# Optimization experiments

Measured on AMD Instinct MI355X. Metric: run time of the kernel, lower is better.

## Reference

```python
import jax, jax.numpy as jnp
import numpy as np

VOCAB, EMBED, ZCH = 4096, 128, 256
B, H, W = 32, 16, 16


def setup_inputs() -> dict:
    key = jax.random.key(0)
    k1, k2, k3, k4 = jax.random.split(key, 4)
    z_e = jax.random.normal(k1, (B, ZCH, H, W), dtype=jnp.float32)
    pre_w = jax.random.normal(k2, (EMBED, ZCH), dtype=jnp.float32) * 0.02
    pre_b = jnp.zeros((EMBED,), dtype=jnp.float32)
    # codebook initialized uniform(-1/vocab, 1/vocab) like the torch module
    emb = jax.random.uniform(k3, (VOCAB, EMBED), dtype=jnp.float32,
                             minval=-1.0 / VOCAB, maxval=1.0 / VOCAB)
    post_w = jax.random.normal(k4, (ZCH, EMBED), dtype=jnp.float32) * 0.02
    post_b = jnp.zeros((ZCH,), dtype=jnp.float32)
    return {"z_e": z_e, "pre_w": pre_w, "pre_b": pre_b, "emb": emb,
            "post_w": post_w, "post_b": post_b}


def reference(z_e, pre_w, pre_b, emb, post_w, post_b):
    # pre_quant_conv: 1x1 conv == per-pixel linear, z_channels -> embed_dim
    z = jnp.einsum('bchw,ec->behw', z_e, pre_w) + pre_b[None, :, None, None]
    b, e, h, w = z.shape
    zf = z.transpose(0, 2, 3, 1).reshape(-1, e)                 # (b*h*w, e)
    # squared distance to all codebook vectors: |z|^2 + |c|^2 - 2 z.c
    dist = (jnp.sum(zf * zf, axis=1, keepdims=True)
            + jnp.sum(emb * emb, axis=1)
            - 2.0 * zf @ emb.T)                                  # (b*h*w, vocab)
    tokens = jnp.argmin(dist, axis=-1)                           # (b*h*w,)
    z_q = emb[tokens].reshape(b, h, w, e).transpose(0, 3, 1, 2)  # (b,e,h,w)
    # straight-through estimator
    dec_in = z + jax.lax.stop_gradient(z_q - z)
    # post_quant_conv: 1x1 conv embed_dim -> z_channels (decoder input)
    rec = jnp.einsum('behw,ce->bchw', dec_in, post_w) + post_b[None, :, None, None]
    return z, z_q, rec
```

## Files before the change

### kernel.cpp

```cpp
#include <hip/hip_runtime.h>
#include <hip/hip_bf16.h>
#include <cstdint>

#define NB   32
#define NC   256
#define NE   128
#define NS   256
#define NV   4096
#define NP   8192
#define NSPLIT 8

typedef unsigned short ushort_t;
typedef __attribute__((ext_vector_type(8))) short bf16x8;
typedef __attribute__((ext_vector_type(8))) unsigned short us8;
typedef __attribute__((ext_vector_type(4))) float f32x4;

__device__ __forceinline__ ushort_t f2bf(float f) {
    __hip_bfloat16 h = __float2bfloat16(f);
    ushort_t u; __builtin_memcpy(&u, &h, 2); return u;
}
__device__ __forceinline__ unsigned asu(float f) { unsigned u; __builtin_memcpy(&u,&f,4); return u; }
__device__ __forceinline__ float    asf(unsigned u) { float f; __builtin_memcpy(&f,&u,4); return f; }

__global__ __launch_bounds__(256) void pack_emb(
    const float* __restrict__ emb, ushort_t* __restrict__ Bpack,
    float* __restrict__ cnorm)
{
    const int t = threadIdx.x;
    const int v     = blockIdx.x * 32 + (t >> 3);
    const int chunk = t & 7;
    const float4* rp = (const float4*)(emb + (size_t)v * NE + chunk * 16);
    float4 x0 = rp[0], x1 = rp[1], x2 = rp[2], x3 = rp[3];
    float xs[16] = { x0.x, x0.y, x0.z, x0.w, x1.x, x1.y, x1.z, x1.w,
                     x2.x, x2.y, x2.z, x2.w, x3.x, x3.y, x3.z, x3.w };
    us8 h0, h1;
    float nn = 0.f;
#pragma unroll
    for (int j = 0; j < 8; j++) {
        nn = fmaf(xs[j], xs[j], nn);
        h0[j] = f2bf(xs[j]);
    }
#pragma unroll
    for (int j = 0; j < 8; j++) {
        nn = fmaf(xs[8 + j], xs[8 + j], nn);
        h1[j] = f2bf(xs[8 + j]);
    }
    nn += __shfl_xor(nn, 1);
    nn += __shfl_xor(nn, 2);
    nn += __shfl_xor(nn, 4);
    if (chunk == 0) cnorm[v] = 0.5f * nn;

    const int G  = v >> 4;
    const int ks = chunk >> 1;
    const int q0 = (chunk & 1) * 2;
    const int L0 = (v & 15) | (q0 << 4);
    const int L1 = (v & 15) | ((q0 + 1) << 4);
    *(us8*)(Bpack + ((size_t)G * 4 + ks) * 512 + L0 * 8) = h0;
    *(us8*)(Bpack + ((size_t)G * 4 + ks) * 512 + L1 * 8) = h1;
}

#define ZE_STR  36
#define ZL_STR  132
#define ZE_OFF  0
#define R1_OFF  0
#define R2_OFF  16896
#define ZL_OFF  36864
#define T4B_OFF 53760
#define CAND_OFF 57856
#define TOK_OFF 61952
#define SM_SIZE 62080

__global__ __launch_bounds__(512, 2) void vq_main(
    const float* __restrict__ z_e, const float* __restrict__ pre_w,
    const float* __restrict__ pre_b, const float* __restrict__ emb,
    const float* __restrict__ post_w, const float* __restrict__ post_b,
    const ushort_t* __restrict__ Bpack, const float* __restrict__ cnorm,
    float* __restrict__ out_z, float* __restrict__ out_zq,
    float* __restrict__ out_rec)
{
    __shared__ __align__(16) char smraw[SM_SIZE];
    float* ze   = (float*)(smraw + ZE_OFF);
    float* r1   = (float*)(smraw + R1_OFF);
    float* r2   = (float*)(smraw + R2_OFF);
    float* zl   = (float*)(smraw + ZL_OFF);
    float* eg   = (float*)(smraw + ZL_OFF);
    float* t4b  = (float*)(smraw + T4B_OFF);
    int*   cand = (int*)(smraw + CAND_OFF);
    int*   tok  = (int*)(smraw + TOK_OFF);

    const int t  = threadIdx.x;
    const int b  = blockIdx.x >> 3;
    const int s0 = (blockIdx.x & 7) * 32;

    for (int idx = t; idx < NC * 32; idx += 512) {
        int c = idx >> 5, i = idx & 31;
        ze[c * ZE_STR + i] = z_e[((size_t)b * NC + c) * NS + s0 + i];
    }
    __syncthreads();

    {
        const int pg = t >> 7;
        const int e  = t & 127;
        const float* wr = pre_w + (size_t)e * NC;
        float a0 = 0.f, a1 = 0.f, a2 = 0.f, a3 = 0.f;
        float a4 = 0.f, a5 = 0.f, a6 = 0.f, a7 = 0.f;
#pragma unroll 2
        for (int c = 0; c < NC; c += 4) {
            float4 w4 = *(const float4*)(wr + c);
            float4 za, zb;
            za = *(const float4*)&ze[(c + 0) * ZE_STR + pg * 8];
            zb = *(const float4*)&ze[(c + 0) * ZE_STR + pg * 8 + 4];
            a0 = fmaf(w4.x, za.x, a0); a1 = fmaf(w4.x, za.y, a1);
            a2 = fmaf(w4.x, za.z, a2); a3 = fmaf(w4.x, za.w, a3);
            a4 = fmaf(w4.x, zb.x, a4); a5 = fmaf(w4.x, zb.y, a5);
            a6 = fmaf(w4.x, zb.z, a6); a7 = fmaf(w4.x, zb.w, a7);
            za = *(const float4*)&ze[(c + 1) * ZE_STR + pg * 8];
            zb = *(const float4*)&ze[(c + 1) * ZE_STR + pg * 8 + 4];
            a0 = fmaf(w4.y, za.x, a0); a1 = fmaf(w4.y, za.y, a1);
            a2 = fmaf(w4.y, za.z, a2); a3 = fmaf(w4.y, za.w, a3);
            a4 = fmaf(w4.y, zb.x, a4); a5 = fmaf(w4.y, zb.y, a5);
            a6 = fmaf(w4.y, zb.z, a6); a7 = fmaf(w4.y, zb.w, a7);
            za = *(const float4*)&ze[(c + 2) * ZE_STR + pg * 8];
            zb = *(const float4*)&ze[(c + 2) * ZE_STR + pg * 8 + 4];
            a0 = fmaf(w4.z, za.x, a0); a1 = fmaf(w4.z, za.y, a1);
            a2 = fmaf(w4.z, za.z, a2); a3 = fmaf(w4.z, za.w, a3);
            a4 = fmaf(w4.z, zb.x, a4); a5 = fmaf(w4.z, zb.y, a5);
            a6 = fmaf(w4.z, zb.z, a6); a7 = fmaf(w4.z, zb.w, a7);
            za = *(const float4*)&ze[(c + 3) * ZE_STR + pg * 8];
            zb = *(const float4*)&ze[(c + 3) * ZE_STR + pg * 8 + 4];
            a0 = fmaf(w4.w, za.x, a0); a1 = fmaf(w4.w, za.y, a1);
            a2 = fmaf(w4.w, za.z, a2); a3 = fmaf(w4.w, za.w, a3);
            a4 = fmaf(w4.w, zb.x, a4); a5 = fmaf(w4.w, zb.y, a5);
            a6 = fmaf(w4.w, zb.z, a6); a7 = fmaf(w4.w, zb.w, a7);
        }
        const float bias = pre_b[e];
        a0 += bias; a1 += bias; a2 += bias; a3 += bias;
        a4 += bias; a5 += bias; a6 += bias; a7 += bias;
        zl[(pg * 8 + 0) * ZL_STR + e] = a0;
        zl[(pg * 8 + 1) * ZL_STR + e] = a1;
        zl[(pg * 8 + 2) * ZL_STR + e] = a2;
        zl[(pg * 8 + 3) * ZL_STR + e] = a3;
        zl[(pg * 8 + 4) * ZL_STR + e] = a4;
        zl[(pg * 8 + 5) * ZL_STR + e] = a5;
        zl[(pg * 8 + 6) * ZL_STR + e] = a6;
        zl[(pg * 8 + 7) * ZL_STR + e] = a7;
        float4 lo = { a0, a1, a2, a3 };
        float4 hi = { a4, a5, a6, a7 };
        float* dst = out_z + ((size_t)b * NE + e) * NS + s0 + pg * 8;
        *(float4*)(dst + 0) = lo;
        *(float4*)(dst + 4) = hi;
    }
    __syncthreads();

    const int wave = t >> 6, lane = t & 63;
    const int am = lane & 15, aq = lane >> 4;

    bf16x8 ah[2][4];
#pragma unroll
    for (int mt = 0; mt < 2; mt++)
#pragma unroll
        for (int ks = 0; ks < 4; ks++) {
            const unsigned* src = (const unsigned*)(zl + (mt * 16 + am) * ZL_STR + ks * 32 + aq * 8);
            union { unsigned u[4]; bf16x8 v; } pk;
#pragma unroll
            for (int pr = 0; pr < 4; pr++)
                pk.u[pr] = (src[2 * pr + 1] & 0xFFFF0000u) | (src[2 * pr] >> 16);
            ah[mt][ks] = pk.v;
        }

    const int wq = wave >> 2;
    const int wv = wave & 3;

    for (int sp = 0; sp < NSPLIT; sp += 2) {
        const int split = sp + wq;
        const int Gbase = split * 32 + wv * 8;
        float cn[8];
#pragma unroll
        for (int cgi = 0; cgi < 8; cgi++)
            cn[cgi] = cnorm[(Gbase + cgi) * 16 + am];

        float b1v[8], b2v[8];
#pragma unroll
        for (int i = 0; i < 8; i++) { b1v[i] = -1e30f; b2v[i] = -1e30f; }

        bf16x8 bh[4], bhn[4];
#pragma unroll
        for (int ks = 0; ks < 4; ks++)
            bh[ks] = *(const bf16x8*)(Bpack + ((size_t)Gbase * 4 + ks) * 512 + lane * 8);

        for (int cgi = 0; cgi < 8; cgi++) {
            if (cgi < 7) {
#pragma unroll
                for (int ks = 0; ks < 4; ks++)
                    bhn[ks] = *(const bf16x8*)(Bpack + ((size_t)(Gbase + cgi + 1) * 4 + ks) * 512 + lane * 8);
            }
            f32x4 acc[2];
#pragma unroll
            for (int mt = 0; mt < 2; mt++) acc[mt] = (f32x4){0.f, 0.f, 0.f, 0.f};
#pragma unroll
            for (int ks = 0; ks < 4; ks++)
#pragma unroll
                for (int mt = 0; mt < 2; mt++)
                    acc[mt] = __builtin_amdgcn_mfma_f32_16x16x32_bf16(ah[mt][ks], bh[ks], acc[mt], 0, 0, 0);

#pragma unroll
            for (int mt = 0; mt < 2; mt++)
#pragma unroll
                for (int reg = 0; reg < 4; reg++) {
                    const int si = mt * 4 + reg;
                    float sc = acc[mt][reg] - cn[cgi];
                    float ev = asf((asu(sc) & ~7u) | (unsigned)cgi);
                    b2v[si] = fmaxf(b2v[si], fminf(ev, b1v[si]));
                    b1v[si] = fmaxf(b1v[si], ev);
                }
#pragma unroll
            for (int ks = 0; ks < 4; ks++) bh[ks] = bhn[ks];
        }

        const int slot = wv * 16 + am;
#pragma unroll
        for (int mt = 0; mt < 2; mt++)
#pragma unroll
            for (int reg = 0; reg < 4; reg++) {
                int px = mt * 16 + aq * 4 + reg;
                r1[(wq * 64 + slot) * 33 + px] = b1v[mt * 4 + reg];
                r2[(wq * 64 + slot) * 33 + px] = b2v[mt * 4 + reg];
            }
        __syncthreads();

        if (t < 256) {
            const int wq2 = t >> 7, rem = t & 127;
            const int px = rem >> 2, ch = rem & 3;
            float t1 = -1e30f, t2 = -1e30f, t3 = -1e30f, t4 = -1e30f;
            for (int i = 0; i < 16; i++) {
                int sl = ch * 16 + i;
#pragma unroll
                for (int e = 0; e < 2; e++) {
                    float raw = e ? r2[(wq2 * 64 + sl) * 33 + px]
                                  : r1[(wq2 * 64 + sl) * 33 + px];
                    unsigned vb = asu(raw);
                    float v = asf((vb & ~511u) | ((unsigned)sl << 3) | (vb & 7u));
                    t4 = fmaxf(t4, fminf(v, t3));
                    t3 = fmaxf(t3, fminf(v, t2));
                    t2 = fmaxf(t2, fminf(v, t1));
                    t1 = fmaxf(t1, v);
                }
            }
            float* dst = t4b + ((wq2 * 32 + px) * 4 + ch) * 4;
            dst[0] = t1; dst[1] = t2; dst[2] = t3; dst[3] = t4;
        }
        __syncthreads();

        if (t < 64) {
            const int wq2 = t >> 5, px = t & 31;
            float u1 = -1e30f, u2 = -1e30f, u3 = -1e30f, u4 = -1e30f;
            for (int ch = 0; ch < 4; ch++) {
#pragma unroll
                for (int j = 0; j < 4; j++) {
                    float v = t4b[((wq2 * 32 + px) * 4 + ch) * 4 + j];
                    u4 = fmaxf(u4, fminf(v, u3));
                    u3 = fmaxf(u3, fminf(v, u2));
                    u2 = fmaxf(u2, fminf(v, u1));
                    u1 = fmaxf(u1, v);
                }
            }
            const int spw = sp + wq2;
            float uu[4] = { u1, u2, u3, u4 };
#pragma unroll
            for (int j = 0; j < 4; j++) {
                unsigned bits = asu(uu[j]) & 511u;
                int w = (int)(bits >> 7), res = (int)((bits >> 3) & 15u), cg = (int)(bits & 7u);
                cand[(spw * 32 + px) * 4 + j] = spw * 512 + (w * 8 + cg) * 16 + res;
            }
        }
        __syncthreads();
    }

    {
        const int il = t >> 4;
        const int cc = t & 15;
        double bs = -1e300; int bi = 0x7fffffff;
        const float* zr = zl + il * ZL_STR;
#pragma unroll
        for (int jj = 0; jj < 2; jj++) {
            int c2 = cc * 2 + jj;
            int split = c2 >> 2, slot = c2 & 3;
            int idx = cand[(split * 32 + il) * 4 + slot];
            const float* er = emb + (size_t)idx * NE;
            double d0 = 0.0, d1 = 0.0, d2 = 0.0, d3 = 0.0;
            double n0 = 0.0, n1 = 0.0, n2 = 0.0, n3 = 0.0;
#pragma unroll
            for (int k = 0; k < NE; k += 16) {
                float4 e0 = *(const float4*)(er + k + 0);
                float4 e1 = *(const float4*)(er + k + 4);
                float4 e2 = *(const float4*)(er + k + 8);
                float4 e3 = *(const float4*)(er + k + 12);
                float4 z0 = *(const float4*)(zr + k + 0);
                float4 z1 = *(const float4*)(zr + k + 4);
                float4 z2 = *(const float4*)(zr + k + 8);
                float4 z3 = *(const float4*)(zr + k + 12);
                d0 += (double)z0.x * e0.x; d0 += (double)z0.y * e0.y;
                d0 += (double)z0.z * e0.z; d0 += (double)z0.w * e0.w;
                d1 += (double)z1.x * e1.x; d1 += (double)z1.y * e1.y;
                d1 += (double)z1.z * e1.z; d1 += (double)z1.w * e1.w;
                d2 += (double)z2.x * e2.x; d2 += (double)z2.y * e2.y;
                d2 += (double)z2.z * e2.z; d2 += (double)z2.w * e2.w;
                d3 += (double)z3.x * e3.x; d3 += (double)z3.y * e3.y;
                d3 += (double)z3.z * e3.z; d3 += (double)z3.w * e3.w;
                n0 += (double)e0.x * e0.x; n0 += (double)e0.y * e0.y;
                n0 += (double)e0.z * e0.z; n0 += (double)e0.w * e0.w;
                n1 += (double)e1.x * e1.x; n1 += (double)e1.y * e1.y;
                n1 += (double)e1.z * e1.z; n1 += (double)e1.w * e1.w;
                n2 += (double)e2.x * e2.x; n2 += (double)e2.y * e2.y;
                n2 += (double)e2.z * e2.z; n2 += (double)e2.w * e2.w;
                n3 += (double)e3.x * e3.x; n3 += (double)e3.y * e3.y;
                n3 += (double)e3.z * e3.z; n3 += (double)e3.w * e3.w;
            }
            double sc = ((d0 + d1) + (d2 + d3)) - 0.5 * ((n0 + n1) + (n2 + n3));
            if (sc > bs || (sc == bs && idx < bi)) { bs = sc; bi = idx; }
        }
#pragma unroll
        for (int m = 1; m <= 8; m <<= 1) {
            double osc = __shfl_xor(bs, m);
            int    obi = __shfl_xor(bi, m);
            if (osc > bs || (osc == bs && obi < bi)) { bs = osc; bi = obi; }
        }
        if (cc == 0) tok[il] = bi;
    }
    __syncthreads();

    for (int idx = t; idx < 32 * 32; idx += 512) {
        int px = idx >> 5, eq = idx & 31;
        float4 v4 = *(const float4*)(emb + (size_t)tok[px] * NE + eq * 4);
        *(float4*)&eg[px * ZL_STR + eq * 4] = v4;
    }
    __syncthreads();
    for (int idx = t; idx < NE * 32; idx += 512) {
        int e = idx >> 5, i = idx & 31;
        out_zq[((size_t)b * NE + e) * NS + s0 + i] = eg[i * ZL_STR + e];
    }
    __syncthreads();

    {
        const int c  = t & 255;
        const int ph = t >> 8;
        const float* wr = post_w + (size_t)c * NE;
        const float bias = post_b[c];
#pragma unroll
        for (int pass = 0; pass < 2; pass++) {
            const int pb = pass * 16 + ph * 8;
            float a0 = 0.f, a1 = 0.f, a2 = 0.f, a3 = 0.f;
            float a4 = 0.f, a5 = 0.f, a6 = 0.f, a7 = 0.f;
#pragma unroll 4
            for (int k = 0; k < NE; k += 4) {
                float4 w4 = *(const float4*)(wr + k);
                float4 q;
                q = *(const float4*)&eg[(pb + 0) * ZL_STR + k];
                a0 = fmaf(w4.x, q.x, fmaf(w4.y, q.y, fmaf(w4.z, q.z, fmaf(w4.w, q.w, a0))));
                q = *(const float4*)&eg[(pb + 1) * ZL_STR + k];
                a1 = fmaf(w4.x, q.x, fmaf(w4.y, q.y, fmaf(w4.z, q.z, fmaf(w4.w, q.w, a1))));
                q = *(const float4*)&eg[(pb + 2) * ZL_STR + k];
                a2 = fmaf(w4.x, q.x, fmaf(w4.y, q.y, fmaf(w4.z, q.z, fmaf(w4.w, q.w, a2))));
                q = *(const float4*)&eg[(pb + 3) * ZL_STR + k];
                a3 = fmaf(w4.x, q.x, fmaf(w4.y, q.y, fmaf(w4.z, q.z, fmaf(w4.w, q.w, a3))));
                q = *(const float4*)&eg[(pb + 4) * ZL_STR + k];
                a4 = fmaf(w4.x, q.x, fmaf(w4.y, q.y, fmaf(w4.z, q.z, fmaf(w4.w, q.w, a4))));
                q = *(const float4*)&eg[(pb + 5) * ZL_STR + k];
                a5 = fmaf(w4.x, q.x, fmaf(w4.y, q.y, fmaf(w4.z, q.z, fmaf(w4.w, q.w, a5))));
                q = *(const float4*)&eg[(pb + 6) * ZL_STR + k];
                a6 = fmaf(w4.x, q.x, fmaf(w4.y, q.y, fmaf(w4.z, q.z, fmaf(w4.w, q.w, a6))));
                q = *(const float4*)&eg[(pb + 7) * ZL_STR + k];
                a7 = fmaf(w4.x, q.x, fmaf(w4.y, q.y, fmaf(w4.z, q.z, fmaf(w4.w, q.w, a7))));
            }
            float4 lo = { a0 + bias, a1 + bias, a2 + bias, a3 + bias };
            float4 hi = { a4 + bias, a5 + bias, a6 + bias, a7 + bias };
            float* dst = out_rec + ((size_t)b * NC + c) * NS + s0 + pb;
            *(float4*)(dst + 0) = lo;
            *(float4*)(dst + 4) = hi;
        }
    }
}

extern "C" void kernel_launch(void* const* d_in, const int* in_sizes, int n_in,
                              void* d_out, int out_size, void* d_ws, size_t ws_size,
                              hipStream_t stream)
{
    const float* z_e    = (const float*)d_in[0];
    const float* pre_w  = (const float*)d_in[1];
    const float* pre_b  = (const float*)d_in[2];
    const float* emb    = (const float*)d_in[3];
    const float* post_w = (const float*)d_in[4];
    const float* post_b = (const float*)d_in[5];

    float* out     = (float*)d_out;
    float* out_z   = out;
    float* out_zq  = out + 1048576;
    float* out_rec = out + 2097152;

    const size_t SZ_BPACK = (size_t)256 * 4 * 512 * 2;
    const size_t SZ_CNORM = (size_t)NV * 4;
    const size_t NEED = SZ_BPACK + SZ_CNORM;
    char* scr = (ws_size >= NEED) ? (char*)d_ws : (char*)out_rec;
    ushort_t* Bpack = (ushort_t*)scr;
    float*    cnorm = (float*)(scr + SZ_BPACK);

    pack_emb<<<dim3(128), 256, 0, stream>>>(emb, Bpack, cnorm);
    vq_main <<<dim3(256), 512, 0, stream>>>(z_e, pre_w, pre_b, emb,
                                            post_w, post_b, Bpack, cnorm,
                                            out_z, out_zq, out_rec);
}
```

Baseline: 144.4 us.

## Halve per-block pixel tile to 16 and double grid to fill more CUs

Each block now handles 16 spatial positions instead of 32, and the grid doubles to 512 blocks. The MFMA codebook scan uses a single M-tile per wave, the shared-memory reduction buffers shrink, and the candidate rerank assigns one candidate per thread. The goal is more parallelism and occupancy across CUs, at the cost of reading the packed codebook twice as often and less operand reuse per MFMA. One barrier between the z_q store and the post-conv is removed.

```diff
diff --git a/kernel.cpp b/kernel.cpp
--- a/kernel.cpp
+++ b/kernel.cpp
@@ -59,16 +59,16 @@
     *(us8*)(Bpack + ((size_t)G * 4 + ks) * 512 + L1 * 8) = h1;
 }
 
-#define ZE_STR  36
-#define ZL_STR  132
-#define ZE_OFF  0
-#define R1_OFF  0
-#define R2_OFF  16896
-#define ZL_OFF  36864
-#define T4B_OFF 53760
-#define CAND_OFF 57856
-#define TOK_OFF 61952
-#define SM_SIZE 62080
+#define ZE_STR   20
+#define ZL_STR   132
+#define ZE_OFF   0
+#define R1_OFF   0
+#define R2_OFF   8704
+#define T4B_OFF  17408
+#define ZL_OFF   20480
+#define CAND_OFF 28928
+#define TOK_OFF  30976
+#define SM_SIZE  31040
 
 __global__ __launch_bounds__(512, 2) void vq_main(
     const float* __restrict__ z_e, const float* __restrict__ pre_w,
@@ -82,19 +82,20 @@
     float* ze   = (float*)(smraw + ZE_OFF);
     float* r1   = (float*)(smraw + R1_OFF);
     float* r2   = (float*)(smraw + R2_OFF);
+    float* t4b  = (float*)(smraw + T4B_OFF);
     float* zl   = (float*)(smraw + ZL_OFF);
     float* eg   = (float*)(smraw + ZL_OFF);
-    float* t4b  = (float*)(smraw + T4B_OFF);
     int*   cand = (int*)(smraw + CAND_OFF);
     int*   tok  = (int*)(smraw + TOK_OFF);
 
     const int t  = threadIdx.x;
-    const int b  = blockIdx.x >> 3;
-    const int s0 = (blockIdx.x & 7) * 32;
-
-    for (int idx = t; idx < NC * 32; idx += 512) {
-        int c = idx >> 5, i = idx & 31;
-        ze[c * ZE_STR + i] = z_e[((size_t)b * NC + c) * NS + s0 + i];
+    const int b  = blockIdx.x >> 4;
+    const int s0 = (blockIdx.x & 15) * 16;
+
+    for (int idx = t; idx < NC * 4; idx += 512) {
+        int c = idx >> 2, q = idx & 3;
+        *(float4*)&ze[c * ZE_STR + q * 4] =
+            *(const float4*)(z_e + ((size_t)b * NC + c) * NS + s0 + q * 4);
     }
     __syncthreads();
 
@@ -103,70 +104,47 @@
         const int e  = t & 127;
         const float* wr = pre_w + (size_t)e * NC;
         float a0 = 0.f, a1 = 0.f, a2 = 0.f, a3 = 0.f;
-        float a4 = 0.f, a5 = 0.f, a6 = 0.f, a7 = 0.f;
 #pragma unroll 2
         for (int c = 0; c < NC; c += 4) {
             float4 w4 = *(const float4*)(wr + c);
-            float4 za, zb;
-            za = *(const float4*)&ze[(c + 0) * ZE_STR + pg * 8];
-            zb = *(const float4*)&ze[(c + 0) * ZE_STR + pg * 8 + 4];
-            a0 = fmaf(w4.x, za.x, a0); a1 = fmaf(w4.x, za.y, a1);
-            a2 = fmaf(w4.x, za.z, a2); a3 = fmaf(w4.x, za.w, a3);
-            a4 = fmaf(w4.x, zb.x, a4); a5 = fmaf(w4.x, zb.y, a5);
-            a6 = fmaf(w4.x, zb.z, a6); a7 = fmaf(w4.x, zb.w, a7);
-            za = *(const float4*)&ze[(c + 1) * ZE_STR + pg * 8];
-            zb = *(const float4*)&ze[(c + 1) * ZE_STR + pg * 8 + 4];
-            a0 = fmaf(w4.y, za.x, a0); a1 = fmaf(w4.y, za.y, a1);
-            a2 = fmaf(w4.y, za.z, a2); a3 = fmaf(w4.y, za.w, a3);
-            a4 = fmaf(w4.y, zb.x, a4); a5 = fmaf(w4.y, zb.y, a5);
-            a6 = fmaf(w4.y, zb.z, a6); a7 = fmaf(w4.y, zb.w, a7);
-            za = *(const float4*)&ze[(c + 2) * ZE_STR + pg * 8];
-            zb = *(const float4*)&ze[(c + 2) * ZE_STR + pg * 8 + 4];
-            a0 = fmaf(w4.z, za.x, a0); a1 = fmaf(w4.z, za.y, a1);
-            a2 = fmaf(w4.z, za.z, a2); a3 = fmaf(w4.z, za.w, a3);
-            a4 = fmaf(w4.z, zb.x, a4); a5 = fmaf(w4.z, zb.y, a5);
-            a6 = fmaf(w4.z, zb.z, a6); a7 = fmaf(w4.z, zb.w, a7);
-            za = *(const float4*)&ze[(c + 3) * ZE_STR + pg * 8];
-            zb = *(const float4*)&ze[(c + 3) * ZE_STR + pg * 8 + 4];
-            a0 = fmaf(w4.w, za.x, a0); a1 = fmaf(w4.w, za.y, a1);
-            a2 = fmaf(w4.w, za.z, a2); a3 = fmaf(w4.w, za.w, a3);
-            a4 = fmaf(w4.w, zb.x, a4); a5 = fmaf(w4.w, zb.y, a5);
-            a6 = fmaf(w4.w, zb.z, a6); a7 = fmaf(w4.w, zb.w, a7);
+            float4 z4;
+            z4 = *(const float4*)&ze[(c + 0) * ZE_STR + pg * 4];
+            a0 = fmaf(w4.x, z4.x, a0); a1 = fmaf(w4.x, z4.y, a1);
+            a2 = fmaf(w4.x, z4.z, a2); a3 = fmaf(w4.x, z4.w, a3);
+            z4 = *(const float4*)&ze[(c + 1) * ZE_STR + pg * 4];
+            a0 = fmaf(w4.y, z4.x, a0); a1 = fmaf(w4.y, z4.y, a1);
+            a2 = fmaf(w4.y, z4.z, a2); a3 = fmaf(w4.y, z4.w, a3);
+            z4 = *(const float4*)&ze[(c + 2) * ZE_STR + pg * 4];
+            a0 = fmaf(w4.z, z4.x, a0); a1 = fmaf(w4.z, z4.y, a1);
+            a2 = fmaf(w4.z, z4.z, a2); a3 = fmaf(w4.z, z4.w, a3);
+            z4 = *(const float4*)&ze[(c + 3) * ZE_STR + pg * 4];
+            a0 = fmaf(w4.w, z4.x, a0); a1 = fmaf(w4.w, z4.y, a1);
+            a2 = fmaf(w4.w, z4.z, a2); a3 = fmaf(w4.w, z4.w, a3);
         }
         const float bias = pre_b[e];
         a0 += bias; a1 += bias; a2 += bias; a3 += bias;
-        a4 += bias; a5 += bias; a6 += bias; a7 += bias;
-        zl[(pg * 8 + 0) * ZL_STR + e] = a0;
-        zl[(pg * 8 + 1) * ZL_STR + e] = a1;
-        zl[(pg * 8 + 2) * ZL_STR + e] = a2;
-        zl[(pg * 8 + 3) * ZL_STR + e] = a3;
-        zl[(pg * 8 + 4) * ZL_STR + e] = a4;
-        zl[(pg * 8 + 5) * ZL_STR + e] = a5;
-        zl[(pg * 8 + 6) * ZL_STR + e] = a6;
-        zl[(pg * 8 + 7) * ZL_STR + e] = a7;
-        float4 lo = { a0, a1, a2, a3 };
-        float4 hi = { a4, a5, a6, a7 };
-        float* dst = out_z + ((size_t)b * NE + e) * NS + s0 + pg * 8;
-        *(float4*)(dst + 0) = lo;
-        *(float4*)(dst + 4) = hi;
+        zl[(pg * 4 + 0) * ZL_STR + e] = a0;
+        zl[(pg * 4 + 1) * ZL_STR + e] = a1;
+        zl[(pg * 4 + 2) * ZL_STR + e] = a2;
+        zl[(pg * 4 + 3) * ZL_STR + e] = a3;
+        float4 o = { a0, a1, a2, a3 };
+        *(float4*)(out_z + ((size_t)b * NE + e) * NS + s0 + pg * 4) = o;
     }
     __syncthreads();
 
     const int wave = t >> 6, lane = t & 63;
     const int am = lane & 15, aq = lane >> 4;
 
-    bf16x8 ah[2][4];
-#pragma unroll
-    for (int mt = 0; mt < 2; mt++)
-#pragma unroll
-        for (int ks = 0; ks < 4; ks++) {
-            const unsigned* src = (const unsigned*)(zl + (mt * 16 + am) * ZL_STR + ks * 32 + aq * 8);
-            union { unsigned u[4]; bf16x8 v; } pk;
-#pragma unroll
-            for (int pr = 0; pr < 4; pr++)
-                pk.u[pr] = (src[2 * pr + 1] & 0xFFFF0000u) | (src[2 * pr] >> 16);
-            ah[mt][ks] = pk.v;
-        }
+    bf16x8 ah[4];
+#pragma unroll
+    for (int ks = 0; ks < 4; ks++) {
+        const unsigned* src = (const unsigned*)(zl + am * ZL_STR + ks * 32 + aq * 8);
+        union { unsigned u[4]; bf16x8 v; } pk;
+#pragma unroll
+        for (int pr = 0; pr < 4; pr++)
+            pk.u[pr] = (src[2 * pr + 1] & 0xFFFF0000u) | (src[2 * pr] >> 16);
+        ah[ks] = pk.v;
+    }
 
     const int wq = wave >> 2;
     const int wv = wave & 3;
@@ -179,9 +157,9 @@
         for (int cgi = 0; cgi < 8; cgi++)
             cn[cgi] = cnorm[(Gbase + cgi) * 16 + am];
 
-        float b1v[8], b2v[8];
-#pragma unroll
-        for (int i = 0; i < 8; i++) { b1v[i] = -1e30f; b2v[i] = -1e30f; }
+        float b1v[4], b2v[4];
+#pragma unroll
+        for (int i = 0; i < 4; i++) { b1v[i] = -1e30f; b2v[i] = -1e30f; }
 
         bf16x8 bh[4], bhn[4];
 #pragma unroll
@@ -194,50 +172,41 @@
                 for (int ks = 0; ks < 4; ks++)
                     bhn[ks] = *(const bf16x8*)(Bpack + ((size_t)(Gbase + cgi + 1) * 4 + ks) * 512 + lane * 8);
             }
-            f32x4 acc[2];
-#pragma unroll
-            for (int mt = 0; mt < 2; mt++) acc[mt] = (f32x4){0.f, 0.f, 0.f, 0.f};
+            f32x4 acc = (f32x4){0.f, 0.f, 0.f, 0.f};
 #pragma unroll
             for (int ks = 0; ks < 4; ks++)
-#pragma unroll
-                for (int mt = 0; mt < 2; mt++)
-                    acc[mt] = __builtin_amdgcn_mfma_f32_16x16x32_bf16(ah[mt][ks], bh[ks], acc[mt], 0, 0, 0);
-
-#pragma unroll
-            for (int mt = 0; mt < 2; mt++)
-#pragma unroll
-                for (int reg = 0; reg < 4; reg++) {
-                    const int si = mt * 4 + reg;
-                    float sc = acc[mt][reg] - cn[cgi];
-                    float ev = asf((asu(sc) & ~7u) | (unsigned)cgi);
-                    b2v[si] = fmaxf(b2v[si], fminf(ev, b1v[si]));
-                    b1v[si] = fmaxf(b1v[si], ev);
-                }
+                acc = __builtin_amdgcn_mfma_f32_16x16x32_bf16(ah[ks], bh[ks], acc, 0, 0, 0);
+
+#pragma unroll
+            for (int reg = 0; reg < 4; reg++) {
+                float sc = acc[reg] - cn[cgi];
+                float ev = asf((asu(sc) & ~7u) | (unsigned)cgi);
+                b2v[reg] = fmaxf(b2v[reg], fminf(ev, b1v[reg]));
+                b1v[reg] = fmaxf(b1v[reg], ev);
+            }
 #pragma unroll
             for (int ks = 0; ks < 4; ks++) bh[ks] = bhn[ks];
         }
 
         const int slot = wv * 16 + am;
 #pragma unroll
-        for (int mt = 0; mt < 2; mt++)
-#pragma unroll
-            for (int reg = 0; reg < 4; reg++) {
-                int px = mt * 16 + aq * 4 + reg;
-                r1[(wq * 64 + slot) * 33 + px] = b1v[mt * 4 + reg];
-                r2[(wq * 64 + slot) * 33 + px] = b2v[mt * 4 + reg];
-            }
+        for (int reg = 0; reg < 4; reg++) {
+            int px = aq * 4 + reg;
+            r1[(wq * 64 + slot) * 17 + px] = b1v[reg];
+            r2[(wq * 64 + slot) * 17 + px] = b2v[reg];
+        }
         __syncthreads();
 
-        if (t < 256) {
-            const int wq2 = t >> 7, rem = t & 127;
+        if (t < 128) {
+            const int wq2 = t >> 6, rem = t & 63;
             const int px = rem >> 2, ch = rem & 3;
             float t1 = -1e30f, t2 = -1e30f, t3 = -1e30f, t4 = -1e30f;
             for (int i = 0; i < 16; i++) {
                 int sl = ch * 16 + i;
 #pragma unroll
                 for (int e = 0; e < 2; e++) {
-                    float raw = e ? r2[(wq2 * 64 + sl) * 33 + px]
-                                  : r1[(wq2 * 64 + sl) * 33 + px];
+                    float raw = e ? r2[(wq2 * 64 + sl) * 17 + px]
+                                  : r1[(wq2 * 64 + sl) * 17 + px];
                     unsigned vb = asu(raw);
                     float v = asf((vb & ~511u) | ((unsigned)sl << 3) | (vb & 7u));
                     t4 = fmaxf(t4, fminf(v, t3));
@@ -246,18 +215,18 @@
                     t1 = fmaxf(t1, v);
                 }
             }
-            float* dst = t4b + ((wq2 * 32 + px) * 4 + ch) * 4;
+            float* dst = t4b + ((wq2 * 16 + px) * 4 + ch) * 4;
             dst[0] = t1; dst[1] = t2; dst[2] = t3; dst[3] = t4;
         }
         __syncthreads();
 
-        if (t < 64) {
-            const int wq2 = t >> 5, px = t & 31;
+        if (t < 32) {
+            const int wq2 = t >> 4, px = t & 15;
             float u1 = -1e30f, u2 = -1e30f, u3 = -1e30f, u4 = -1e30f;
             for (int ch = 0; ch < 4; ch++) {
 #pragma unroll
                 for (int j = 0; j < 4; j++) {
-                    float v = t4b[((wq2 * 32 + px) * 4 + ch) * 4 + j];
+                    float v = t4b[((wq2 * 16 + px) * 4 + ch) * 4 + j];
                     u4 = fmaxf(u4, fminf(v, u3));
                     u3 = fmaxf(u3, fminf(v, u2));
                     u2 = fmaxf(u2, fminf(v, u1));
@@ -270,57 +239,53 @@
             for (int j = 0; j < 4; j++) {
                 unsigned bits = asu(uu[j]) & 511u;
                 int w = (int)(bits >> 7), res = (int)((bits >> 3) & 15u), cg = (int)(bits & 7u);
-                cand[(spw * 32 + px) * 4 + j] = spw * 512 + (w * 8 + cg) * 16 + res;
+                cand[(spw * 16 + px) * 4 + j] = spw * 512 + (w * 8 + cg) * 16 + res;
             }
         }
         __syncthreads();
     }
 
     {
-        const int il = t >> 4;
-        const int cc = t & 15;
-        double bs = -1e300; int bi = 0x7fffffff;
+        const int il = t >> 5;
+        const int cc = t & 31;
+        const int split = cc >> 2, slot = cc & 3;
+        const int idx = cand[(split * 16 + il) * 4 + slot];
+        const float* er = emb + (size_t)idx * NE;
         const float* zr = zl + il * ZL_STR;
-#pragma unroll
-        for (int jj = 0; jj < 2; jj++) {
-            int c2 = cc * 2 + jj;
-            int split = c2 >> 2, slot = c2 & 3;
-            int idx = cand[(split * 32 + il) * 4 + slot];
-            const float* er = emb + (size_t)idx * NE;
-            double d0 = 0.0, d1 = 0.0, d2 = 0.0, d3 = 0.0;
-            double n0 = 0.0, n1 = 0.0, n2 = 0.0, n3 = 0.0;
-#pragma unroll
-            for (int k = 0; k < NE; k += 16) {
-                float4 e0 = *(const float4*)(er + k + 0);
-                float4 e1 = *(const float4*)(er + k + 4);
-                float4 e2 = *(const float4*)(er + k + 8);
-                float4 e3 = *(const float4*)(er + k + 12);
-                float4 z0 = *(const float4*)(zr + k + 0);
-                float4 z1 = *(const float4*)(zr + k + 4);
-                float4 z2 = *(const float4*)(zr + k + 8);
-                float4 z3 = *(const float4*)(zr + k + 12);
-                d0 += (double)z0.x * e0.x; d0 += (double)z0.y * e0.y;
-                d0 += (double)z0.z * e0.z; d0 += (double)z0.w * e0.w;
-                d1 += (double)z1.x * e1.x; d1 += (double)z1.y * e1.y;
-                d1 += (double)z1.z * e1.z; d1 += (double)z1.w * e1.w;
-                d2 += (double)z2.x * e2.x; d2 += (double)z2.y * e2.y;
-                d2 += (double)z2.z * e2.z; d2 += (double)z2.w * e2.w;
-                d3 += (double)z3.x * e3.x; d3 += (double)z3.y * e3.y;
-                d3 += (double)z3.z * e3.z; d3 += (double)z3.w * e3.w;
-                n0 += (double)e0.x * e0.x; n0 += (double)e0.y * e0.y;
-                n0 += (double)e0.z * e0.z; n0 += (double)e0.w * e0.w;
-                n1 += (double)e1.x * e1.x; n1 += (double)e1.y * e1.y;
-                n1 += (double)e1.z * e1.z; n1 += (double)e1.w * e1.w;
-                n2 += (double)e2.x * e2.x; n2 += (double)e2.y * e2.y;
-                n2 += (double)e2.z * e2.z; n2 += (double)e2.w * e2.w;
-                n3 += (double)e3.x * e3.x; n3 += (double)e3.y * e3.y;
-                n3 += (double)e3.z * e3.z; n3 += (double)e3.w * e3.w;
-            }
-            double sc = ((d0 + d1) + (d2 + d3)) - 0.5 * ((n0 + n1) + (n2 + n3));
-            if (sc > bs || (sc == bs && idx < bi)) { bs = sc; bi = idx; }
-        }
-#pragma unroll
-        for (int m = 1; m <= 8; m <<= 1) {
+
+        double d0 = 0.0, d1 = 0.0, d2 = 0.0, d3 = 0.0;
+        double n0 = 0.0, n1 = 0.0, n2 = 0.0, n3 = 0.0;
+#pragma unroll
+        for (int k = 0; k < NE; k += 16) {
+            float4 e0 = *(const float4*)(er + k + 0);
+            float4 e1 = *(const float4*)(er + k + 4);
+            float4 e2 = *(const float4*)(er + k + 8);
+            float4 e3 = *(const float4*)(er + k + 12);
+            float4 z0 = *(const float4*)(zr + k + 0);
+            float4 z1 = *(const float4*)(zr + k + 4);
+            float4 z2 = *(const float4*)(zr + k + 8);
+            float4 z3 = *(const float4*)(zr + k + 12);
+            d0 += (double)z0.x * e0.x; d0 += (double)z0.y * e0.y;
+            d0 += (double)z0.z * e0.z; d0 += (double)z0.w * e0.w;
+            d1 += (double)z1.x * e1.x; d1 += (double)z1.y * e1.y;
+            d1 += (double)z1.z * e1.z; d1 += (double)z1.w * e1.w;
+            d2 += (double)z2.x * e2.x; d2 += (double)z2.y * e2.y;
+            d2 += (double)z2.z * e2.z; d2 += (double)z2.w * e2.w;
+            d3 += (double)z3.x * e3.x; d3 += (double)z3.y * e3.y;
+            d3 += (double)z3.z * e3.z; d3 += (double)z3.w * e3.w;
+            n0 += (double)e0.x * e0.x; n0 += (double)e0.y * e0.y;
+            n0 += (double)e0.z * e0.z; n0 += (double)e0.w * e0.w;
+            n1 += (double)e1.x * e1.x; n1 += (double)e1.y * e1.y;
+            n1 += (double)e1.z * e1.z; n1 += (double)e1.w * e1.w;
+            n2 += (double)e2.x * e2.x; n2 += (double)e2.y * e2.y;
+            n2 += (double)e2.z * e2.z; n2 += (double)e2.w * e2.w;
+            n3 += (double)e3.x * e3.x; n3 += (double)e3.y * e3.y;
+            n3 += (double)e3.z * e3.z; n3 += (double)e3.w * e3.w;
+        }
+        double bs = ((d0 + d1) + (d2 + d3)) - 0.5 * ((n0 + n1) + (n2 + n3));
+        int bi = idx;
+#pragma unroll
+        for (int m = 1; m <= 16; m <<= 1) {
             double osc = __shfl_xor(bs, m);
             int    obi = __shfl_xor(bi, m);
             if (osc > bs || (osc == bs && obi < bi)) { bs = osc; bi = obi; }
@@ -329,55 +294,51 @@
     }
     __syncthreads();
 
-    for (int idx = t; idx < 32 * 32; idx += 512) {
-        int px = idx >> 5, eq = idx & 31;
-        float4 v4 = *(const float4*)(emb + (size_t)tok[px] * NE + eq * 4);
-        *(float4*)&eg[px * ZL_STR + eq * 4] = v4;
+    {
+        const int px = t >> 5, eq = t & 31;
+        *(float4*)&eg[px * ZL_STR + eq * 4] =
+            *(const float4*)(emb + (size_t)tok[px] * NE + eq * 4);
     }
     __syncthreads();
-    for (int idx = t; idx < NE * 32; idx += 512) {
-        int e = idx >> 5, i = idx & 31;
+    for (int idx = t; idx < NE * 16; idx += 512) {
+        int e = idx >> 4, i = idx & 15;
         out_zq[((size_t)b * NE + e) * NS + s0 + i] = eg[i * ZL_STR + e];
     }
-    __syncthreads();
 
     {
         const int c  = t & 255;
         const int ph = t >> 8;
+        const int pb = ph * 8;
         const float* wr = post_w + (size_t)c * NE;
         const float bias = post_b[c];
-#pragma unroll
-        for (int pass = 0; pass < 2; pass++) {
-            const int pb = pass * 16 + ph * 8;
-            float a0 = 0.f, a1 = 0.f, a2 = 0.f, a3 = 0.f;
-            float a4 = 0.f, a5 = 0.f, a6 = 0.f, a7 = 0.f;
+        float a0 = 0.f, a1 = 0.f, a2 = 0.f, a3 = 0.f;
+        float a4 = 0.f, a5 = 0.f, a6 = 0.f, a7 = 0.f;
 #pragma unroll 4
-            for (int k = 0; k < NE; k += 4) {
-                float4 w4 = *(const float4*)(wr + k);
-                float4 q;
-                q = *(const float4*)&eg[(pb + 0) * ZL_STR + k];
-                a0 = fmaf(w4.x, q.x, fmaf(w4.y, q.y, fmaf(w4.z, q.z, fmaf(w4.w, q.w, a0))));
-                q = *(const float4*)&eg[(pb + 1) * ZL_STR + k];
-                a1 = fmaf(w4.x, q.x, fmaf(w4.y, q.y, fmaf(w4.z, q.z, fmaf(w4.w, q.w, a1))));
-                q = *(const float4*)&eg[(pb + 2) * ZL_STR + k];
-                a2 = fmaf(w4.x, q.x, fmaf(w4.y, q.y, fmaf(w4.z, q.z, fmaf(w4.w, q.w, a2))));
-                q = *(const float4*)&eg[(pb + 3) * ZL_STR + k];
-                a3 = fmaf(w4.x, q.x, fmaf(w4.y, q.y, fmaf(w4.z, q.z, fmaf(w4.w, q.w, a3))));
-                q = *(const float4*)&eg[(pb + 4) * ZL_STR + k];
-                a4 = fmaf(w4.x, q.x, fmaf(w4.y, q.y, fmaf(w4.z, q.z, fmaf(w4.w, q.w, a4))));
-                q = *(const float4*)&eg[(pb + 5) * ZL_STR + k];
-                a5 = fmaf(w4.x, q.x, fmaf(w4.y, q.y, fmaf(w4.z, q.z, fmaf(w4.w, q.w, a5))));
-                q = *(const float4*)&eg[(pb + 6) * ZL_STR + k];
-                a6 = fmaf(w4.x, q.x, fmaf(w4.y, q.y, fmaf(w4.z, q.z, fmaf(w4.w, q.w, a6))));
-                q = *(const float4*)&eg[(pb + 7) * ZL_STR + k];
-                a7 = fmaf(w4.x, q.x, fmaf(w4.y, q.y, fmaf(w4.z, q.z, fmaf(w4.w, q.w, a7))));
-            }
-            float4 lo = { a0 + bias, a1 + bias, a2 + bias, a3 + bias };
-            float4 hi = { a4 + bias, a5 + bias, a6 + bias, a7 + bias };
-            float* dst = out_rec + ((size_t)b * NC + c) * NS + s0 + pb;
-            *(float4*)(dst + 0) = lo;
-            *(float4*)(dst + 4) = hi;
-        }
+        for (int k = 0; k < NE; k += 4) {
+            float4 w4 = *(const float4*)(wr + k);
+            float4 q;
+            q = *(const float4*)&eg[(pb + 0) * ZL_STR + k];
+            a0 = fmaf(w4.x, q.x, fmaf(w4.y, q.y, fmaf(w4.z, q.z, fmaf(w4.w, q.w, a0))));
+            q = *(const float4*)&eg[(pb + 1) * ZL_STR + k];
+            a1 = fmaf(w4.x, q.x, fmaf(w4.y, q.y, fmaf(w4.z, q.z, fmaf(w4.w, q.w, a1))));
+            q = *(const float4*)&eg[(pb + 2) * ZL_STR + k];
+            a2 = fmaf(w4.x, q.x, fmaf(w4.y, q.y, fmaf(w4.z, q.z, fmaf(w4.w, q.w, a2))));
+            q = *(const float4*)&eg[(pb + 3) * ZL_STR + k];
+            a3 = fmaf(w4.x, q.x, fmaf(w4.y, q.y, fmaf(w4.z, q.z, fmaf(w4.w, q.w, a3))));
+            q = *(const float4*)&eg[(pb + 4) * ZL_STR + k];
+            a4 = fmaf(w4.x, q.x, fmaf(w4.y, q.y, fmaf(w4.z, q.z, fmaf(w4.w, q.w, a4))));
+            q = *(const float4*)&eg[(pb + 5) * ZL_STR + k];
+            a5 = fmaf(w4.x, q.x, fmaf(w4.y, q.y, fmaf(w4.z, q.z, fmaf(w4.w, q.w, a5))));
+            q = *(const float4*)&eg[(pb + 6) * ZL_STR + k];
+            a6 = fmaf(w4.x, q.x, fmaf(w4.y, q.y, fmaf(w4.z, q.z, fmaf(w4.w, q.w, a6))));
+            q = *(const float4*)&eg[(pb + 7) * ZL_STR + k];
+            a7 = fmaf(w4.x, q.x, fmaf(w4.y, q.y, fmaf(w4.z, q.z, fmaf(w4.w, q.w, a7))));
+        }
+        float4 lo = { a0 + bias, a1 + bias, a2 + bias, a3 + bias };
+        float4 hi = { a4 + bias, a5 + bias, a6 + bias, a7 + bias };
+        float* dst = out_rec + ((size_t)b * NC + c) * NS + s0 + pb;
+        *(float4*)(dst + 0) = lo;
+        *(float4*)(dst + 4) = hi;
     }
 }
 
@@ -405,7 +366,7 @@
     float*    cnorm = (float*)(scr + SZ_BPACK);
 
     pack_emb<<<dim3(128), 256, 0, stream>>>(emb, Bpack, cnorm);
-    vq_main <<<dim3(256), 512, 0, stream>>>(z_e, pre_w, pre_b, emb,
+    vq_main <<<dim3(512), 512, 0, stream>>>(z_e, pre_w, pre_b, emb,
                                             post_w, post_b, Bpack, cnorm,
                                             out_z, out_zq, out_rec);
 }
```

After: 180.7 us. 25.2% more time.

## Split VQ kernel into front and back kernels with global candidate buffer

Applied to the files above, without the earlier changes.

Splits the fused kernel into vq_front (pre-conv, bf16 distance search, top-4 candidates per split written to a global buffer) and vq_back (fp64 rescoring, gather, post-conv). vq_back runs 512 blocks of 16 pixels with higher occupancy, one candidate per lane, so the tail stages get more parallelism than the 256-block fused kernel gave them. The cost is an extra launch plus global round trips for z and the candidate indices. If the workspace is too small the scratch falls back to out_rec, which vq_back also writes.

```diff
diff --git a/kernel.cpp b/kernel.cpp
--- a/kernel.cpp
+++ b/kernel.cpp
@@ -66,27 +66,20 @@
 #define R2_OFF  16896
 #define ZL_OFF  36864
 #define T4B_OFF 53760
-#define CAND_OFF 57856
-#define TOK_OFF 61952
-#define SM_SIZE 62080
-
-__global__ __launch_bounds__(512, 2) void vq_main(
+#define SM_SIZE 57856
+
+__global__ __launch_bounds__(512, 2) void vq_front(
     const float* __restrict__ z_e, const float* __restrict__ pre_w,
-    const float* __restrict__ pre_b, const float* __restrict__ emb,
-    const float* __restrict__ post_w, const float* __restrict__ post_b,
+    const float* __restrict__ pre_b,
     const ushort_t* __restrict__ Bpack, const float* __restrict__ cnorm,
-    float* __restrict__ out_z, float* __restrict__ out_zq,
-    float* __restrict__ out_rec)
+    float* __restrict__ out_z, int* __restrict__ pidx4)
 {
     __shared__ __align__(16) char smraw[SM_SIZE];
     float* ze   = (float*)(smraw + ZE_OFF);
     float* r1   = (float*)(smraw + R1_OFF);
     float* r2   = (float*)(smraw + R2_OFF);
     float* zl   = (float*)(smraw + ZL_OFF);
-    float* eg   = (float*)(smraw + ZL_OFF);
     float* t4b  = (float*)(smraw + T4B_OFF);
-    int*   cand = (int*)(smraw + CAND_OFF);
-    int*   tok  = (int*)(smraw + TOK_OFF);
 
     const int t  = threadIdx.x;
     const int b  = blockIdx.x >> 3;
@@ -265,62 +258,82 @@
                 }
             }
             const int spw = sp + wq2;
+            const int p = blockIdx.x * 32 + px;
             float uu[4] = { u1, u2, u3, u4 };
 #pragma unroll
             for (int j = 0; j < 4; j++) {
                 unsigned bits = asu(uu[j]) & 511u;
                 int w = (int)(bits >> 7), res = (int)((bits >> 3) & 15u), cg = (int)(bits & 7u);
-                cand[(spw * 32 + px) * 4 + j] = spw * 512 + (w * 8 + cg) * 16 + res;
+                pidx4[((size_t)spw * NP + p) * 4 + j] = spw * 512 + (w * 8 + cg) * 16 + res;
             }
         }
         __syncthreads();
     }
+}
+
+__global__ __launch_bounds__(512, 4) void vq_back(
+    const float* __restrict__ z, const float* __restrict__ emb,
+    const int* __restrict__ pidx4, const float* __restrict__ post_w,
+    const float* __restrict__ post_b, float* __restrict__ out_zq,
+    float* __restrict__ out_rec)
+{
+    __shared__ __align__(16) float zl[16 * 132];
+    __shared__ __align__(16) float eg[16 * 132];
+    __shared__ int tok[16];
+
+    const int t  = threadIdx.x;
+    const int p0 = blockIdx.x * 16;
+    const int b  = p0 >> 8;
+    const int s0 = p0 & 255;
+
+    for (int idx = t; idx < 16 * 128; idx += 512) {
+        int k = idx >> 4, i = idx & 15;
+        zl[i * 132 + k] = z[(size_t)(b * NE + k) * NS + s0 + i];
+    }
+    __syncthreads();
 
     {
-        const int il = t >> 4;
-        const int cc = t & 15;
-        double bs = -1e300; int bi = 0x7fffffff;
-        const float* zr = zl + il * ZL_STR;
-#pragma unroll
-        for (int jj = 0; jj < 2; jj++) {
-            int c2 = cc * 2 + jj;
-            int split = c2 >> 2, slot = c2 & 3;
-            int idx = cand[(split * 32 + il) * 4 + slot];
-            const float* er = emb + (size_t)idx * NE;
-            double d0 = 0.0, d1 = 0.0, d2 = 0.0, d3 = 0.0;
-            double n0 = 0.0, n1 = 0.0, n2 = 0.0, n3 = 0.0;
-#pragma unroll
-            for (int k = 0; k < NE; k += 16) {
-                float4 e0 = *(const float4*)(er + k + 0);
-                float4 e1 = *(const float4*)(er + k + 4);
-                float4 e2 = *(const float4*)(er + k + 8);
-                float4 e3 = *(const float4*)(er + k + 12);
-                float4 z0 = *(const float4*)(zr + k + 0);
-                float4 z1 = *(const float4*)(zr + k + 4);
-                float4 z2 = *(const float4*)(zr + k + 8);
-                float4 z3 = *(const float4*)(zr + k + 12);
-                d0 += (double)z0.x * e0.x; d0 += (double)z0.y * e0.y;
-                d0 += (double)z0.z * e0.z; d0 += (double)z0.w * e0.w;
-                d1 += (double)z1.x * e1.x; d1 += (double)z1.y * e1.y;
-                d1 += (double)z1.z * e1.z; d1 += (double)z1.w * e1.w;
-                d2 += (double)z2.x * e2.x; d2 += (double)z2.y * e2.y;
-                d2 += (double)z2.z * e2.z; d2 += (double)z2.w * e2.w;
-                d3 += (double)z3.x * e3.x; d3 += (double)z3.y * e3.y;
-                d3 += (double)z3.z * e3.z; d3 += (double)z3.w * e3.w;
-                n0 += (double)e0.x * e0.x; n0 += (double)e0.y * e0.y;
-                n0 += (double)e0.z * e0.z; n0 += (double)e0.w * e0.w;
-                n1 += (double)e1.x * e1.x; n1 += (double)e1.y * e1.y;
-                n1 += (double)e1.z * e1.z; n1 += (double)e1.w * e1.w;
-                n2 += (double)e2.x * e2.x; n2 += (double)e2.y * e2.y;
-                n2 += (double)e2.z * e2.z; n2 += (double)e2.w * e2.w;
-                n3 += (double)e3.x * e3.x; n3 += (double)e3.y * e3.y;
-                n3 += (double)e3.z * e3.z; n3 += (double)e3.w * e3.w;
-            }
-            double sc = ((d0 + d1) + (d2 + d3)) - 0.5 * ((n0 + n1) + (n2 + n3));
-            if (sc > bs || (sc == bs && idx < bi)) { bs = sc; bi = idx; }
-        }
-#pragma unroll
-        for (int m = 1; m <= 8; m <<= 1) {
+        const int il = t >> 5;
+        const int cc = t & 31;
+        const int p  = p0 + il;
+        const int split = cc >> 2, slot = cc & 3;
+        const int idx = pidx4[((size_t)split * NP + p) * 4 + slot];
+        const float* er = emb + (size_t)idx * NE;
+        const float* zr = &zl[il * 132];
+
+        double d0 = 0.0, d1 = 0.0, d2 = 0.0, d3 = 0.0;
+        double n0 = 0.0, n1 = 0.0, n2 = 0.0, n3 = 0.0;
+#pragma unroll
+        for (int k = 0; k < NE; k += 16) {
+            float4 e0 = *(const float4*)(er + k + 0);
+            float4 e1 = *(const float4*)(er + k + 4);
+            float4 e2 = *(const float4*)(er + k + 8);
+            float4 e3 = *(const float4*)(er + k + 12);
+            float4 z0 = *(const float4*)(zr + k + 0);
+            float4 z1 = *(const float4*)(zr + k + 4);
+            float4 z2 = *(const float4*)(zr + k + 8);
+            float4 z3 = *(const float4*)(zr + k + 12);
+            d0 += (double)z0.x * e0.x; d0 += (double)z0.y * e0.y;
+            d0 += (double)z0.z * e0.z; d0 += (double)z0.w * e0.w;
+            d1 += (double)z1.x * e1.x; d1 += (double)z1.y * e1.y;
+            d1 += (double)z1.z * e1.z; d1 += (double)z1.w * e1.w;
+            d2 += (double)z2.x * e2.x; d2 += (double)z2.y * e2.y;
+            d2 += (double)z2.z * e2.z; d2 += (double)z2.w * e2.w;
+            d3 += (double)z3.x * e3.x; d3 += (double)z3.y * e3.y;
+            d3 += (double)z3.z * e3.z; d3 += (double)z3.w * e3.w;
+            n0 += (double)e0.x * e0.x; n0 += (double)e0.y * e0.y;
+            n0 += (double)e0.z * e0.z; n0 += (double)e0.w * e0.w;
+            n1 += (double)e1.x * e1.x; n1 += (double)e1.y * e1.y;
+            n1 += (double)e1.z * e1.z; n1 += (double)e1.w * e1.w;
+            n2 += (double)e2.x * e2.x; n2 += (double)e2.y * e2.y;
+            n2 += (double)e2.z * e2.z; n2 += (double)e2.w * e2.w;
+            n3 += (double)e3.x * e3.x; n3 += (double)e3.y * e3.y;
+            n3 += (double)e3.z * e3.z; n3 += (double)e3.w * e3.w;
+        }
+        double bs = ((d0 + d1) + (d2 + d3)) - 0.5 * ((n0 + n1) + (n2 + n3));
+        int bi = idx;
+#pragma unroll
+        for (int m = 1; m <= 16; m <<= 1) {
             double osc = __shfl_xor(bs, m);
             int    obi = __shfl_xor(bi, m);
             if (osc > bs || (osc == bs && obi < bi)) { bs = osc; bi = obi; }
@@ -329,55 +342,49 @@
     }
     __syncthreads();
 
-    for (int idx = t; idx < 32 * 32; idx += 512) {
-        int px = idx >> 5, eq = idx & 31;
-        float4 v4 = *(const float4*)(emb + (size_t)tok[px] * NE + eq * 4);
-        *(float4*)&eg[px * ZL_STR + eq * 4] = v4;
-    }
-    __syncthreads();
-    for (int idx = t; idx < NE * 32; idx += 512) {
-        int e = idx >> 5, i = idx & 31;
-        out_zq[((size_t)b * NE + e) * NS + s0 + i] = eg[i * ZL_STR + e];
+    for (int idx = t; idx < NE * 16; idx += 512) {
+        int e = idx >> 4, i = idx & 15;
+        float v = emb[(size_t)tok[i] * NE + e];
+        out_zq[(size_t)(b * NE + e) * NS + s0 + i] = v;
+        eg[i * 132 + e] = v;
     }
     __syncthreads();
 
     {
         const int c  = t & 255;
         const int ph = t >> 8;
+        const int pb = ph * 8;
         const float* wr = post_w + (size_t)c * NE;
+
+        float a0 = 0.f, a1 = 0.f, a2 = 0.f, a3 = 0.f;
+        float a4 = 0.f, a5 = 0.f, a6 = 0.f, a7 = 0.f;
+#pragma unroll 4
+        for (int k = 0; k < NE; k += 4) {
+            float4 w4 = *(const float4*)(wr + k);
+            float4 q;
+            q = *(const float4*)&eg[(pb + 0) * 132 + k];
+            a0 = fmaf(w4.x, q.x, fmaf(w4.y, q.y, fmaf(w4.z, q.z, fmaf(w4.w, q.w, a0))));
+            q = *(const float4*)&eg[(pb + 1) * 132 + k];
+            a1 = fmaf(w4.x, q.x, fmaf(w4.y, q.y, fmaf(w4.z, q.z, fmaf(w4.w, q.w, a1))));
+            q = *(const float4*)&eg[(pb + 2) * 132 + k];
+            a2 = fmaf(w4.x, q.x, fmaf(w4.y, q.y, fmaf(w4.z, q.z, fmaf(w4.w, q.w, a2))));
+            q = *(const float4*)&eg[(pb + 3) * 132 + k];
+            a3 = fmaf(w4.x, q.x, fmaf(w4.y, q.y, fmaf(w4.z, q.z, fmaf(w4.w, q.w, a3))));
+            q = *(const float4*)&eg[(pb + 4) * 132 + k];
+            a4 = fmaf(w4.x, q.x, fmaf(w4.y, q.y, fmaf(w4.z, q.z, fmaf(w4.w, q.w, a4))));
+            q = *(const float4*)&eg[(pb + 5) * 132 + k];
+            a5 = fmaf(w4.x, q.x, fmaf(w4.y, q.y, fmaf(w4.z, q.z, fmaf(w4.w, q.w, a5))));
+            q = *(const float4*)&eg[(pb + 6) * 132 + k];
+            a6 = fmaf(w4.x, q.x, fmaf(w4.y, q.y, fmaf(w4.z, q.z, fmaf(w4.w, q.w, a6))));
+            q = *(const float4*)&eg[(pb + 7) * 132 + k];
+            a7 = fmaf(w4.x, q.x, fmaf(w4.y, q.y, fmaf(w4.z, q.z, fmaf(w4.w, q.w, a7))));
+        }
         const float bias = post_b[c];
-#pragma unroll
-        for (int pass = 0; pass < 2; pass++) {
-            const int pb = pass * 16 + ph * 8;
-            float a0 = 0.f, a1 = 0.f, a2 = 0.f, a3 = 0.f;
-            float a4 = 0.f, a5 = 0.f, a6 = 0.f, a7 = 0.f;
-#pragma unroll 4
-            for (int k = 0; k < NE; k += 4) {
-                float4 w4 = *(const float4*)(wr + k);
-                float4 q;
-                q = *(const float4*)&eg[(pb + 0) * ZL_STR + k];
-                a0 = fmaf(w4.x, q.x, fmaf(w4.y, q.y, fmaf(w4.z, q.z, fmaf(w4.w, q.w, a0))));
-                q = *(const float4*)&eg[(pb + 1) * ZL_STR + k];
-                a1 = fmaf(w4.x, q.x, fmaf(w4.y, q.y, fmaf(w4.z, q.z, fmaf(w4.w, q.w, a1))));
-                q = *(const float4*)&eg[(pb + 2) * ZL_STR + k];
-                a2 = fmaf(w4.x, q.x, fmaf(w4.y, q.y, fmaf(w4.z, q.z, fmaf(w4.w, q.w, a2))));
-                q = *(const float4*)&eg[(pb + 3) * ZL_STR + k];
-                a3 = fmaf(w4.x, q.x, fmaf(w4.y, q.y, fmaf(w4.z, q.z, fmaf(w4.w, q.w, a3))));
-                q = *(const float4*)&eg[(pb + 4) * ZL_STR + k];
-                a4 = fmaf(w4.x, q.x, fmaf(w4.y, q.y, fmaf(w4.z, q.z, fmaf(w4.w, q.w, a4))));
-                q = *(const float4*)&eg[(pb + 5) * ZL_STR + k];
-                a5 = fmaf(w4.x, q.x, fmaf(w4.y, q.y, fmaf(w4.z, q.z, fmaf(w4.w, q.w, a5))));
-                q = *(const float4*)&eg[(pb + 6) * ZL_STR + k];
-                a6 = fmaf(w4.x, q.x, fmaf(w4.y, q.y, fmaf(w4.z, q.z, fmaf(w4.w, q.w, a6))));
-                q = *(const float4*)&eg[(pb + 7) * ZL_STR + k];
-                a7 = fmaf(w4.x, q.x, fmaf(w4.y, q.y, fmaf(w4.z, q.z, fmaf(w4.w, q.w, a7))));
-            }
-            float4 lo = { a0 + bias, a1 + bias, a2 + bias, a3 + bias };
-            float4 hi = { a4 + bias, a5 + bias, a6 + bias, a7 + bias };
-            float* dst = out_rec + ((size_t)b * NC + c) * NS + s0 + pb;
-            *(float4*)(dst + 0) = lo;
-            *(float4*)(dst + 4) = hi;
-        }
+        float4 lo = { a0 + bias, a1 + bias, a2 + bias, a3 + bias };
+        float4 hi = { a4 + bias, a5 + bias, a6 + bias, a7 + bias };
+        float* dst = out_rec + (size_t)(b * NC + c) * NS + s0 + pb;
+        *(float4*)(dst + 0) = lo;
+        *(float4*)(dst + 4) = hi;
     }
 }
 
@@ -399,13 +406,16 @@
 
     const size_t SZ_BPACK = (size_t)256 * 4 * 512 * 2;
     const size_t SZ_CNORM = (size_t)NV * 4;
-    const size_t NEED = SZ_BPACK + SZ_CNORM;
+    const size_t SZ_PIDX4 = (size_t)NSPLIT * NP * 4 * 4;
+    const size_t NEED = SZ_BPACK + SZ_CNORM + SZ_PIDX4;
     char* scr = (ws_size >= NEED) ? (char*)d_ws : (char*)out_rec;
     ushort_t* Bpack = (ushort_t*)scr;
     float*    cnorm = (float*)(scr + SZ_BPACK);
+    int*      pidx4 = (int*)(scr + SZ_BPACK + SZ_CNORM);
 
     pack_emb<<<dim3(128), 256, 0, stream>>>(emb, Bpack, cnorm);
-    vq_main <<<dim3(256), 512, 0, stream>>>(z_e, pre_w, pre_b, emb,
-                                            post_w, post_b, Bpack, cnorm,
-                                            out_z, out_zq, out_rec);
+    vq_front<<<dim3(256), 512, 0, stream>>>(z_e, pre_w, pre_b, Bpack, cnorm,
+                                            out_z, pidx4);
+    vq_back <<<dim3(512), 512, 0, stream>>>(out_z, emb, pidx4,
+                                            post_w, post_b, out_zq, out_rec);
 }
```

New measurement: 149.3 us. +3.4%, slower.
